# Performance work log

Hardware: AMD Instinct MI355X
Metric: run time of the kernel (lower is better)

Reference implementation:

```python
import jax, jax.numpy as jnp
import numpy as np

B, M, H = 1024, 32, 2
D = 64
N_ENT = 500000
N_REL = 32


def setup_inputs() -> dict:
    key = jax.random.key(0)
    k1, k2, k3, k4 = jax.random.split(key, 4)
    edge_index = jax.random.randint(k1, (B, 2), 0, N_ENT, dtype=jnp.int64)
    # column 0: head entity ids, column 1: relation ids; keep both < N_REL so both are in-range
    ripple_sets = jax.random.randint(k2, (H, B, M, 2), 0, N_REL, dtype=jnp.int64)
    entity_emb = jax.random.normal(k3, (N_ENT, D), dtype=jnp.float32)
    relation_emb = jax.random.normal(k4, (N_REL, D * D), dtype=jnp.float32)
    # padding_idx=0 -> row 0 is zeros
    entity_emb = entity_emb.at[0].set(0.0)
    relation_emb = relation_emb.at[0].set(0.0)
    return {
        "edge_index": edge_index,
        "ripple_sets": ripple_sets,
        "entity_emb": entity_emb,
        "relation_emb": relation_emb,
    }


def reference(edge_index, ripple_sets, entity_emb, relation_emb):
    d = entity_emb.shape[1]
    item = entity_emb[edge_index[:, 1]]            # [B, d]
    u = jnp.zeros_like(item)                       # [B, d]
    for hop in range(ripple_sets.shape[0]):        # small fixed hop count
        rs = ripple_sets[hop]                      # [B, M, 2]
        R = relation_emb[rs[:, :, 1]].reshape(rs.shape[0], -1, d, d)  # [B, M, d, d]
        h = entity_emb[rs[:, :, 0]]                # [B, M, d]
        Rh = jnp.einsum('bmij,bmj->bmi', R, h)     # [B, M, d]
        vRh = jnp.einsum('bmi,bi->bm', Rh, item)   # [B, M]
        p = jax.nn.softmax(vRh, axis=1)            # [B, M]
        u = u + jnp.einsum('bm,bmd->bd', p, h)     # weighted sum of tails (t == h)
    return jnp.sum(u * item, axis=1, keepdims=True)  # [B, 1]
```

## Files before the change

### kernel.cpp

```cpp
#include <hip/hip_runtime.h>
#include <math.h>

#define BB   1024
#define MM   32
#define HH   2
#define DD   64
#define NREL 32
#define TBB  32

__global__ __launch_bounds__(256) void compute_q(
    const int* __restrict__ edge_index,
    const float* __restrict__ entity_emb,
    const float* __restrict__ relation_emb,
    float* __restrict__ qout)
{
    __shared__ float R_s[DD * DD];
    __shared__ float item_s[TBB * 68];

    const int r   = blockIdx.y;
    const int b0  = blockIdx.x * TBB;
    const int tid = threadIdx.x;

    const float4* Rg = (const float4*)(relation_emb + (size_t)r * DD * DD);
    #pragma unroll
    for (int k = 0; k < 4; ++k)
        ((float4*)R_s)[tid + 256 * k] = Rg[tid + 256 * k];

    #pragma unroll
    for (int k = 0; k < 2; ++k) {
        int idx = tid + 256 * k;
        int bl  = idx >> 4;
        int c4  = idx & 15;
        int ei  = edge_index[2 * (b0 + bl) + 1];
        ((float4*)(item_s + bl * 68))[c4] =
            *(const float4*)(entity_emb + (size_t)ei * DD + c4 * 4);
    }
    __syncthreads();

    const int j4  = (tid & 15) * 4;
    const int bl0 = tid >> 4;
    float4 acc0 = {0.f, 0.f, 0.f, 0.f};
    float4 acc1 = {0.f, 0.f, 0.f, 0.f};
    #pragma unroll 8
    for (int i = 0; i < DD; ++i) {
        const float4 rv = *(const float4*)(R_s + i * DD + j4);
        const float a0 = item_s[bl0 * 68 + i];
        const float a1 = item_s[(bl0 + 16) * 68 + i];
        acc0.x += a0 * rv.x; acc0.y += a0 * rv.y;
        acc0.z += a0 * rv.z; acc0.w += a0 * rv.w;
        acc1.x += a1 * rv.x; acc1.y += a1 * rv.y;
        acc1.z += a1 * rv.z; acc1.w += a1 * rv.w;
    }
    size_t q0 = ((size_t)(b0 + bl0) * NREL + r) * DD + j4;
    size_t q1 = ((size_t)(b0 + bl0 + 16) * NREL + r) * DD + j4;
    *(float4*)(qout + q0) = acc0;
    *(float4*)(qout + q1) = acc1;
}

#define HS 65

__global__ __launch_bounds__(256) void ripple_apply(
    const int* __restrict__ edge_index,
    const int* __restrict__ ripple_sets,
    const float* __restrict__ entity_emb,
    const float* __restrict__ qg,
    float* __restrict__ out)
{
    __shared__ float item_s[DD];
    __shared__ float h_s[HH * MM * HS];
    __shared__ float q_s[HH * MM * HS];
    __shared__ float vp_s[4 * 64];
    __shared__ float p_s[HH * MM];
    __shared__ float up_s[4 * 68];

    const int b   = blockIdx.x;
    const int tid = threadIdx.x;

    if (tid < DD) {
        int item_idx = edge_index[2 * b + 1];
        item_s[tid] = entity_emb[(size_t)item_idx * DD + tid];
    }

    #pragma unroll
    for (int k = 0; k < 4; ++k) {
        int idx = tid + 256 * k;
        int row = idx >> 4;
        int c4  = idx & 15;
        int hop = row >> 5, m = row & 31;
        size_t ibase = ((size_t)(hop * BB + b) * MM + m) * 2;
        int head = ripple_sets[ibase];
        int rel  = ripple_sets[ibase + 1];
        const float4 hv = *(const float4*)(entity_emb + (size_t)head * DD + c4 * 4);
        float* hd = h_s + row * HS + c4 * 4;
        hd[0] = hv.x; hd[1] = hv.y; hd[2] = hv.z; hd[3] = hv.w;
        const float4 qv = *(const float4*)(qg + ((size_t)b * NREL + rel) * DD + c4 * 4);
        float* qd = q_s + row * HS + c4 * 4;
        qd[0] = qv.x; qd[1] = qv.y; qd[2] = qv.z; qd[3] = qv.w;
    }
    __syncthreads();

    {
        int t = tid & 63;
        int q = tid >> 6;
        const float* qp = q_s + t * HS + q * 16;
        const float* hp = h_s + t * HS + q * 16;
        float acc = 0.f;
        #pragma unroll
        for (int j = 0; j < 16; ++j) acc += qp[j] * hp[j];
        vp_s[q * 64 + t] = acc;
    }
    __syncthreads();

    if (tid < HH * MM) {
        float v = vp_s[tid] + vp_s[64 + tid] + vp_s[128 + tid] + vp_s[192 + tid];
        float mx = v;
        #pragma unroll
        for (int off = 16; off > 0; off >>= 1)
            mx = fmaxf(mx, __shfl_xor(mx, off, 64));
        float e = expf(v - mx);
        float s = e;
        #pragma unroll
        for (int off = 16; off > 0; off >>= 1)
            s += __shfl_xor(s, off, 64);
        p_s[tid] = e / s;
    }
    __syncthreads();

    {
        int d    = tid & 63;
        int part = tid >> 6;
        float u = 0.f;
        #pragma unroll
        for (int tt = 0; tt < 16; ++tt) {
            int t = part * 16 + tt;
            u += p_s[t] * h_s[t * HS + d];
        }
        up_s[part * 68 + d] = u;
    }
    __syncthreads();

    if (tid < DD) {
        float u = up_s[tid] + up_s[68 + tid] + up_s[136 + tid] + up_s[204 + tid];
        float prod = u * item_s[tid];
        #pragma unroll
        for (int off = 32; off > 0; off >>= 1) prod += __shfl_down(prod, off, 64);
        if (tid == 0) out[b] = prod;
    }
}

extern "C" void kernel_launch(void* const* d_in, const int* in_sizes, int n_in,
                              void* d_out, int out_size, void* d_ws, size_t ws_size,
                              hipStream_t stream) {
    const int*   edge_index   = (const int*)d_in[0];
    const int*   ripple_sets  = (const int*)d_in[1];
    const float* entity_emb   = (const float*)d_in[2];
    const float* relation_emb = (const float*)d_in[3];
    float* out = (float*)d_out;
    float* qbuf = (float*)d_ws;
    (void)in_sizes; (void)n_in; (void)out_size; (void)ws_size;

    compute_q<<<dim3(BB / TBB, NREL), dim3(256), 0, stream>>>(
        edge_index, entity_emb, relation_emb, qbuf);
    ripple_apply<<<dim3(BB), dim3(256), 0, stream>>>(
        edge_index, ripple_sets, entity_emb, qbuf, out);
}
```

Measured before the change: 169.8 us.

## Compute ripple scores in registers with shuffles, dropping q shared-memory staging

The ripple_apply kernel now loads h and q rows into registers and computes the per-row dot products directly with 16-lane xor-shuffle reductions. This removes the q_s shared buffer and its store/reload, and merges the score, softmax and weighted-sum phases so two barriers go away. Every wave now computes the softmax redundantly and broadcasts p via shuffles instead of shared memory. Shared memory per block shrinks and launch bounds request 4 blocks per CU, which should raise occupancy at some cost in register pressure.

```diff
diff --git a/kernel.cpp b/kernel.cpp
--- a/kernel.cpp
+++ b/kernel.cpp
@@ -59,7 +59,7 @@
 
 #define HS 65
 
-__global__ __launch_bounds__(256) void ripple_apply(
+__global__ __launch_bounds__(256, 4) void ripple_apply(
     const int* __restrict__ edge_index,
     const int* __restrict__ ripple_sets,
     const float* __restrict__ entity_emb,
@@ -68,82 +68,88 @@
 {
     __shared__ float item_s[DD];
     __shared__ float h_s[HH * MM * HS];
-    __shared__ float q_s[HH * MM * HS];
-    __shared__ float vp_s[4 * 64];
-    __shared__ float p_s[HH * MM];
+    __shared__ float v_s[HH * MM];
     __shared__ float up_s[4 * 68];
 
-    const int b   = blockIdx.x;
-    const int tid = threadIdx.x;
+    const int b    = blockIdx.x;
+    const int tid  = threadIdx.x;
+    const int lane = tid & 63;
+    const int r0   = tid >> 4;
+    const int c4   = tid & 15;
 
+    int head[4], rel[4];
+    #pragma unroll
+    for (int k = 0; k < 4; ++k) {
+        int row = r0 + 16 * k;
+        int hop = row >> 5, m = row & 31;
+        size_t ibase = ((size_t)(hop * BB + b) * MM + m) * 2;
+        head[k] = ripple_sets[ibase];
+        rel[k]  = ripple_sets[ibase + 1];
+    }
     if (tid < DD) {
         int item_idx = edge_index[2 * b + 1];
         item_s[tid] = entity_emb[(size_t)item_idx * DD + tid];
     }
 
+    float4 hv[4], qv[4];
+    #pragma unroll
+    for (int k = 0; k < 4; ++k)
+        hv[k] = *(const float4*)(entity_emb + (size_t)head[k] * DD + c4 * 4);
+    #pragma unroll
+    for (int k = 0; k < 4; ++k)
+        qv[k] = *(const float4*)(qg + ((size_t)b * NREL + rel[k]) * DD + c4 * 4);
+
+    float vp[4];
     #pragma unroll
     for (int k = 0; k < 4; ++k) {
-        int idx = tid + 256 * k;
-        int row = idx >> 4;
-        int c4  = idx & 15;
-        int hop = row >> 5, m = row & 31;
-        size_t ibase = ((size_t)(hop * BB + b) * MM + m) * 2;
-        int head = ripple_sets[ibase];
-        int rel  = ripple_sets[ibase + 1];
-        const float4 hv = *(const float4*)(entity_emb + (size_t)head * DD + c4 * 4);
+        int row = r0 + 16 * k;
         float* hd = h_s + row * HS + c4 * 4;
-        hd[0] = hv.x; hd[1] = hv.y; hd[2] = hv.z; hd[3] = hv.w;
-        const float4 qv = *(const float4*)(qg + ((size_t)b * NREL + rel) * DD + c4 * 4);
-        float* qd = q_s + row * HS + c4 * 4;
-        qd[0] = qv.x; qd[1] = qv.y; qd[2] = qv.z; qd[3] = qv.w;
+        hd[0] = hv[k].x; hd[1] = hv[k].y; hd[2] = hv[k].z; hd[3] = hv[k].w;
+        vp[k] = hv[k].x * qv[k].x + hv[k].y * qv[k].y
+              + hv[k].z * qv[k].z + hv[k].w * qv[k].w;
+    }
+    #pragma unroll
+    for (int off = 1; off < 16; off <<= 1) {
+        #pragma unroll
+        for (int k = 0; k < 4; ++k)
+            vp[k] += __shfl_xor(vp[k], off, 64);
+    }
+    if (c4 == 0) {
+        #pragma unroll
+        for (int k = 0; k < 4; ++k)
+            v_s[r0 + 16 * k] = vp[k];
     }
     __syncthreads();
 
-    {
-        int t = tid & 63;
-        int q = tid >> 6;
-        const float* qp = q_s + t * HS + q * 16;
-        const float* hp = h_s + t * HS + q * 16;
-        float acc = 0.f;
-        #pragma unroll
-        for (int j = 0; j < 16; ++j) acc += qp[j] * hp[j];
-        vp_s[q * 64 + t] = acc;
+    float v  = v_s[lane];
+    float mx = v;
+    #pragma unroll
+    for (int off = 16; off > 0; off >>= 1)
+        mx = fmaxf(mx, __shfl_xor(mx, off, 64));
+    float e = expf(v - mx);
+    float s = e;
+    #pragma unroll
+    for (int off = 16; off > 0; off >>= 1)
+        s += __shfl_xor(s, off, 64);
+    float p = e / s;
+
+    const int w = tid >> 6;
+    float u = 0.f;
+    #pragma unroll
+    for (int tt = 0; tt < 16; ++tt) {
+        int t = w * 16 + tt;
+        float pt = __shfl(p, t, 64);
+        u += pt * h_s[t * HS + lane];
     }
-    __syncthreads();
-
-    if (tid < HH * MM) {
-        float v = vp_s[tid] + vp_s[64 + tid] + vp_s[128 + tid] + vp_s[192 + tid];
-        float mx = v;
-        #pragma unroll
-        for (int off = 16; off > 0; off >>= 1)
-            mx = fmaxf(mx, __shfl_xor(mx, off, 64));
-        float e = expf(v - mx);
-        float s = e;
-        #pragma unroll
-        for (int off = 16; off > 0; off >>= 1)
-            s += __shfl_xor(s, off, 64);
-        p_s[tid] = e / s;
-    }
-    __syncthreads();
-
-    {
-        int d    = tid & 63;
-        int part = tid >> 6;
-        float u = 0.f;
-        #pragma unroll
-        for (int tt = 0; tt < 16; ++tt) {
-            int t = part * 16 + tt;
-            u += p_s[t] * h_s[t * HS + d];
-        }
-        up_s[part * 68 + d] = u;
-    }
+    up_s[w * 68 + lane] = u;
     __syncthreads();
 
     if (tid < DD) {
-        float u = up_s[tid] + up_s[68 + tid] + up_s[136 + tid] + up_s[204 + tid];
-        float prod = u * item_s[tid];
+        float uu = up_s[tid] + up_s[68 + tid] + up_s[136 + tid] + up_s[204 + tid];
+        float prod = uu * item_s[tid];
         #pragma unroll
-        for (int off = 32; off > 0; off >>= 1) prod += __shfl_down(prod, off, 64);
+        for (int off = 32; off > 0; off >>= 1)
+            prod += __shfl_down(prod, off, 64);
         if (tid == 0) out[b] = prod;
     }
 }
```

After: 173.5 us. 2.2% more time.
